# Kernel tuning notes

Hardware: AMD Instinct MI355X
Metric: run time of the kernel (lower is better)

## Reference

```python
import jax, jax.numpy as jnp
import numpy as np

# Graph / model dims (see init_kwargs)
N = 50000          # nodes
E = 800000         # edges (before self loops)
IN, HID, OUT = 128, 64, 47
HEADS = (4, 4, 1)
SLOPE = 0.2        # PyG GATConv default negative_slope
# dropout p=0.6 in the torch module is a no-op in eval mode -> omitted


def _glorot(key, shape):
    fan_in = shape[0] if len(shape) == 2 else int(np.prod(shape))
    return jax.random.normal(key, shape, jnp.float32) / np.sqrt(fan_in)


def setup_inputs() -> dict:
    key = jax.random.key(0)
    ks = jax.random.split(key, 16)
    x = jax.random.normal(ks[0], (N, IN), jnp.float32)
    edge_index = jax.random.randint(ks[1], (2, E), 0, N)
    # layer dims: (in_dim, out_dim_per_head, heads)
    dims = [(IN, HID, HEADS[0]), (HID * HEADS[0], HID, HEADS[1]), (HID * HEADS[1], OUT, HEADS[2])]
    inp = {"x": x, "edge_index": edge_index}
    for i, (d_in, c, h) in enumerate(dims, start=1):
        inp[f"W{i}"] = _glorot(ks[3 * i], (d_in, h * c))
        inp[f"a{i}s"] = _glorot(ks[3 * i + 1], (h, c))
        inp[f"a{i}d"] = _glorot(ks[3 * i + 2], (h, c))
        inp[f"b{i}"] = jnp.zeros((h * c,), jnp.float32)
    return inp


def gat_layer(x, src, dst, W, a_s, a_d, b, h, c):
    # x: [N, d_in] -> per-head features [N, h, c]
    feat = (x @ W).reshape(N, h, c)
    # per-node attention logits [N, h]
    al_src = jnp.einsum('nhc,hc->nh', feat, a_s)
    al_dst = jnp.einsum('nhc,hc->nh', feat, a_d)
    # per-edge score, LeakyReLU (PyG: alpha = a_src[src] + a_dst[dst])
    e = jax.nn.leaky_relu(al_src[src] + al_dst[dst], SLOPE)  # [Etot, h]
    # segment softmax over incoming edges of each dst node
    emax = jax.ops.segment_max(e, dst, num_segments=N)       # [N, h]
    w = jnp.exp(e - emax[dst])
    denom = jax.ops.segment_sum(w, dst, num_segments=N)      # [N, h]
    alpha = w / denom[dst]                                   # [Etot, h]
    # weighted scatter-add aggregation
    out = jax.ops.segment_sum(alpha[:, :, None] * feat[src], dst, num_segments=N)
    return out.reshape(N, h * c) + b                         # concat heads + bias


def reference(x, edge_index, W1, a1s, a1d, b1, W2, a2s, a2d, b2, W3, a3s, a3d, b3):
    loop = jnp.arange(N, dtype=edge_index.dtype)
    src = jnp.concatenate([edge_index[0], loop])  # add_self_loops=True
    dst = jnp.concatenate([edge_index[1], loop])
    h = gat_layer(x, src, dst, W1, a1s, a1d, b1, HEADS[0], HID)
    h = jax.nn.elu(h)
    h = gat_layer(h, src, dst, W2, a2s, a2d, b2, HEADS[1], HID)
    h = jax.nn.elu(h)
    h = gat_layer(h, src, dst, W3, a3s, a3d, b3, HEADS[2], OUT)  # no elu on last layer
    return h
```

## Files before the change

### kernel.cpp

```cpp
#include <hip/hip_runtime.h>
#include <hip/hip_bf16.h>

#define NNODES 50000
#define NEDGES 800000
#define ETOT   (NNODES + NEDGES)
#define MTILES 3136
#define MPAD   (MTILES * 16)
#define NBLK   196

typedef __attribute__((ext_vector_type(8))) short short8;
typedef __attribute__((ext_vector_type(4))) float floatx4;
typedef __attribute__((ext_vector_type(2))) unsigned int uint2v;

__device__ __forceinline__ float bf2f(__hip_bfloat16 x) { return __bfloat162float(x); }
__device__ __forceinline__ __hip_bfloat16 f2bf(float f) { return __float2bfloat16(f); }
__device__ __forceinline__ float sane(float v, float c) {
  v = (v == v) ? v : 0.f;
  return fminf(fmaxf(v, -c), c);
}

__global__ void zero_int_kernel(int* __restrict__ p, int n) {
  int i = blockIdx.x * blockDim.x + threadIdx.x;
  if (i < n) p[i] = 0;
}
__global__ void fill_out_kernel(float* __restrict__ o, int n, float v) {
  int i = blockIdx.x * blockDim.x + threadIdx.x;
  if (i < n) o[i] = v;
}
__global__ void split_input_kernel(const float* __restrict__ in,
                                   __hip_bfloat16* __restrict__ hi,
                                   __hip_bfloat16* __restrict__ lo, int n) {
  int i = blockIdx.x * blockDim.x + threadIdx.x;
  if (i >= n) return;
  float v = sane(in[i], 1e4f);
  __hip_bfloat16 h = f2bf(v);
  hi[i] = h;
  lo[i] = f2bf(v - bf2f(h));
}
__global__ void zero_tail_kernel(__hip_bfloat16* __restrict__ hi,
                                 __hip_bfloat16* __restrict__ lo) {
  const int base = NNODES * 128;
  const int cnt = MPAD * 256 - base;
  int i = blockIdx.x * blockDim.x + threadIdx.x;
  if (i >= cnt) return;
  hi[base + i] = f2bf(0.f);
  lo[base + i] = f2bf(0.f);
}
__global__ void pad47_kernel(const float* __restrict__ a, const float* __restrict__ b,
                             float* __restrict__ ap, float* __restrict__ bp) {
  int i = threadIdx.x;
  ap[i] = (i < 47) ? sane(a[i], 1e4f) : 0.f;
  bp[i] = (i < 47) ? sane(b[i], 1e4f) : 0.f;
}

__global__ void degree_kernel(const int* __restrict__ ei, int* __restrict__ deg) {
  int p = blockIdx.x * blockDim.x + threadIdx.x;
  if (p >= ETOT) return;
  int dst = (p < NEDGES) ? ei[NEDGES + p] : (p - NEDGES);
  dst = min(max(dst, 0), NNODES - 1);
  atomicAdd(&deg[dst], 1);
}

__global__ __launch_bounds__(256) void block_sum_kernel(const int* __restrict__ deg,
                                                        int* __restrict__ bsum) {
  __shared__ int sh[256];
  int b = blockIdx.x, t = threadIdx.x;
  int i = b * 256 + t;
  sh[t] = (i < NNODES) ? deg[i] : 0;
  __syncthreads();
  for (int off = 128; off > 0; off >>= 1) {
    if (t < off) sh[t] += sh[t + off];
    __syncthreads();
  }
  if (t == 0) bsum[b] = sh[0];
}

__global__ __launch_bounds__(256) void scan_bsum_kernel(const int* __restrict__ bsum,
                                                        int* __restrict__ boff,
                                                        int* __restrict__ row_ptr) {
  __shared__ int sh[256];
  int t = threadIdx.x;
  int v = (t < NBLK) ? bsum[t] : 0;
  sh[t] = v;
  __syncthreads();
  for (int off = 1; off < 256; off <<= 1) {
    int u = (t >= off) ? sh[t - off] : 0;
    __syncthreads();
    sh[t] += u;
    __syncthreads();
  }
  if (t < NBLK) boff[t] = sh[t] - v;
  if (t == 255) row_ptr[NNODES] = sh[255];
}

__global__ __launch_bounds__(256) void emit_rowptr_kernel(const int* __restrict__ deg,
                                                          const int* __restrict__ boff,
                                                          int* __restrict__ row_ptr,
                                                          int* __restrict__ cursor) {
  __shared__ int sh[256];
  int b = blockIdx.x, t = threadIdx.x;
  int i = b * 256 + t;
  int d = (i < NNODES) ? deg[i] : 0;
  sh[t] = d;
  __syncthreads();
  for (int off = 1; off < 256; off <<= 1) {
    int u = (t >= off) ? sh[t - off] : 0;
    __syncthreads();
    sh[t] += u;
    __syncthreads();
  }
  if (i < NNODES) {
    int v = boff[b] + sh[t] - d;
    row_ptr[i] = v;
    cursor[i] = v;
  }
}

__global__ void scatter_kernel(const int* __restrict__ ei, int* __restrict__ cursor,
                               int* __restrict__ csr_src) {
  int p = blockIdx.x * blockDim.x + threadIdx.x;
  if (p >= ETOT) return;
  int src, dst;
  if (p < NEDGES) { src = ei[p]; dst = ei[NEDGES + p]; }
  else            { src = p - NEDGES; dst = src; }
  src = min(max(src, 0), NNODES - 1);
  dst = min(max(dst, 0), NNODES - 1);
  int pos = atomicAdd(&cursor[dst], 1);
  pos = min(max(pos, 0), ETOT - 1);
  csr_src[pos] = src;
}

__global__ void pack_w_kernel(const float* __restrict__ W,
                              __hip_bfloat16* __restrict__ Bh,
                              __hip_bfloat16* __restrict__ Bl,
                              int K, int Nreal, int Npad) {
  int idx = blockIdx.x * blockDim.x + threadIdx.x;
  if (idx >= Npad * K) return;
  int e = idx;
  int j = e & 7;    e >>= 3;
  int m = e & 15;   e >>= 4;
  int quad = e & 3; e >>= 2;
  int kch = K >> 5;
  int kk32 = e % kch;
  int nt = e / kch;
  int n = nt * 16 + m;
  int k = kk32 * 32 + quad * 8 + j;
  float v = (n < Nreal) ? sane(W[k * Nreal + n], 1e4f) : 0.f;
  __hip_bfloat16 h = f2bf(v);
  Bh[idx] = h;
  Bl[idx] = f2bf(v - bf2f(h));
}

template<int KDIM, int NOUT, int HEADS, int WAVES_N>
__global__ __launch_bounds__(256) void gemm_attn_kernel(
    const __hip_bfloat16* __restrict__ Ah, const __hip_bfloat16* __restrict__ Al,
    const __hip_bfloat16* __restrict__ Bh, const __hip_bfloat16* __restrict__ Bl,
    const float* __restrict__ asv, const float* __restrict__ adv,
    __hip_bfloat16* __restrict__ Ch, float* __restrict__ als, float* __restrict__ ald) {
  constexpr int KCH = KDIM / 32;
  constexpr int CT = (NOUT / 16) / WAVES_N;
  constexpr int RT = 4;
  constexpr int RGROUPS = 4 / WAVES_N;
  __shared__ __hip_bfloat16 sAh[64 * 32];
  __shared__ __hip_bfloat16 sAl[64 * 32];
  int wave = threadIdx.x >> 6, lane = threadIdx.x & 63;
  int wrow = wave / WAVES_N, wcol = wave % WAVES_N;
  int rt0 = (blockIdx.x * RGROUPS + wrow) * RT;
  int ct0 = wcol * CT;
  int m = lane & 15, quad = lane >> 4;

  const short8* Bph = reinterpret_cast<const short8*>(Bh);
  const short8* Bpl = reinterpret_cast<const short8*>(Bl);

  floatx4 acc[RT][CT];
#pragma unroll
  for (int rt = 0; rt < RT; ++rt)
#pragma unroll
    for (int ct = 0; ct < CT; ++ct) acc[rt][ct] = (floatx4){0.f, 0.f, 0.f, 0.f};

  int tid = threadIdx.x;
  size_t gstage = (size_t)(rt0 * 16 + (tid >> 2)) * KDIM + (tid & 3) * 8;

#pragma unroll 2
  for (int kk = 0; kk < KCH; ++kk) {
    short8 a_h[RT], a_l[RT];
    if constexpr (WAVES_N == 4) {
      short8 vh = *reinterpret_cast<const short8*>(Ah + gstage + kk * 32);
      short8 vl = *reinterpret_cast<const short8*>(Al + gstage + kk * 32);
      __syncthreads();
      *reinterpret_cast<short8*>(&sAh[tid * 8]) = vh;
      *reinterpret_cast<short8*>(&sAl[tid * 8]) = vl;
      __syncthreads();
#pragma unroll
      for (int rt = 0; rt < RT; ++rt) {
        int so = (rt * 16 + m) * 32 + quad * 8;
        a_h[rt] = *reinterpret_cast<const short8*>(&sAh[so]);
        a_l[rt] = *reinterpret_cast<const short8*>(&sAl[so]);
      }
    } else {
#pragma unroll
      for (int rt = 0; rt < RT; ++rt) {
        size_t aoff = (size_t)((rt0 + rt) * 16 + m) * KDIM + kk * 32 + quad * 8;
        a_h[rt] = *reinterpret_cast<const short8*>(Ah + aoff);
        a_l[rt] = *reinterpret_cast<const short8*>(Al + aoff);
      }
    }
#pragma unroll
    for (int ct = 0; ct < CT; ++ct) {
      size_t o = ((size_t)(ct0 + ct) * KCH + kk) * 64 + lane;
      short8 b_h = Bph[o];
      short8 b_l = Bpl[o];
#pragma unroll
      for (int rt = 0; rt < RT; ++rt) {
        acc[rt][ct] = __builtin_amdgcn_mfma_f32_16x16x32_bf16(a_h[rt], b_h, acc[rt][ct], 0, 0, 0);
        acc[rt][ct] = __builtin_amdgcn_mfma_f32_16x16x32_bf16(a_h[rt], b_l, acc[rt][ct], 0, 0, 0);
        acc[rt][ct] = __builtin_amdgcn_mfma_f32_16x16x32_bf16(a_l[rt], b_h, acc[rt][ct], 0, 0, 0);
      }
    }
  }

  constexpr int CPH = NOUT / HEADS;
  int head = (ct0 * 16) / CPH;
  float asl[CT], adl[CT];
#pragma unroll
  for (int ct = 0; ct < CT; ++ct) {
    asl[ct] = asv[(ct0 + ct) * 16 + m];
    adl[ct] = adv[(ct0 + ct) * 16 + m];
  }
  float ps[RT * 4], pd[RT * 4];
#pragma unroll
  for (int i = 0; i < RT * 4; ++i) { ps[i] = 0.f; pd[i] = 0.f; }
#pragma unroll
  for (int rt = 0; rt < RT; ++rt)
#pragma unroll
    for (int ct = 0; ct < CT; ++ct)
#pragma unroll
      for (int r = 0; r < 4; ++r) {
        ps[rt * 4 + r] += acc[rt][ct][r] * asl[ct];
        pd[rt * 4 + r] += acc[rt][ct][r] * adl[ct];
      }
#pragma unroll
  for (int off = 1; off < 16; off <<= 1) {
#pragma unroll
    for (int i = 0; i < RT * 4; ++i) {
      ps[i] += __shfl_xor(ps[i], off);
      pd[i] += __shfl_xor(pd[i], off);
    }
  }
  if (m == 0) {
#pragma unroll
    for (int rt = 0; rt < RT; ++rt)
#pragma unroll
      for (int r = 0; r < 4; ++r) {
        int row = (rt0 + rt) * 16 + quad * 4 + r;
        if (row < NNODES) {
          als[(size_t)row * HEADS + head] = sane(ps[rt * 4 + r], 80.f);
          ald[(size_t)row * HEADS + head] = sane(pd[rt * 4 + r], 80.f);
        }
      }
  }

#pragma unroll
  for (int rt = 0; rt < RT; ++rt)
#pragma unroll
    for (int ct = 0; ct < CT; ++ct)
#pragma unroll
      for (int r = 0; r < 4; ++r) {
        int row = (rt0 + rt) * 16 + quad * 4 + r;
        if (row < NNODES) {
          float v = sane(acc[rt][ct][r], 3e4f);
          Ch[(size_t)row * NOUT + (ct0 + ct) * 16 + m] = f2bf(v);
        }
      }
}

template<int H>
__global__ __launch_bounds__(256) void alpha_kernel(const int* __restrict__ row_ptr,
                                                    const int* __restrict__ csr_src,
                                                    const float* __restrict__ als,
                                                    const float* __restrict__ ald,
                                                    float* __restrict__ alpha) {
  int wid = threadIdx.x >> 6, lane = threadIdx.x & 63;
  int dst = blockIdx.x * 4 + wid;
  if (dst >= NNODES) return;
  int start = row_ptr[dst], end = row_ptr[dst + 1];
  int cnt = end - start;
  if (cnt <= 0) return;
  float adv[H];
#pragma unroll
  for (int h = 0; h < H; ++h) adv[h] = ald[(size_t)dst * H + h];

  if (cnt <= 64) {
    int i = start + lane;
    bool valid = lane < cnt;
    int s = valid ? min(max(csr_src[i], 0), NNODES - 1) : 0;
    float w[H];
#pragma unroll
    for (int h = 0; h < H; ++h) {
      float e = als[(size_t)s * H + h] + adv[h];
      e = e > 0.f ? e : 0.2f * e;
      e = fminf(fmaxf(e, -80.f), 80.f);
      w[h] = valid ? __expf(e) : 0.f;
    }
#pragma unroll
    for (int h = 0; h < H; ++h) {
      float v = w[h];
#pragma unroll
      for (int off = 1; off < 64; off <<= 1) v += __shfl_xor(v, off);
      float inv = 1.f / fmaxf(v, 1e-30f);
      if (valid) alpha[(size_t)i * H + h] = w[h] * inv;
    }
  } else {
    float dl[H];
#pragma unroll
    for (int h = 0; h < H; ++h) dl[h] = 0.f;
    for (int base = start; base < end; base += 64) {
      int i = base + lane;
      bool valid = i < end;
      int s = valid ? min(max(csr_src[i], 0), NNODES - 1) : 0;
#pragma unroll
      for (int h = 0; h < H; ++h) {
        float e = als[(size_t)s * H + h] + adv[h];
        e = e > 0.f ? e : 0.2f * e;
        e = fminf(fmaxf(e, -80.f), 80.f);
        float w = valid ? __expf(e) : 0.f;
        dl[h] += w;
        if (valid) alpha[(size_t)i * H + h] = w;
      }
    }
    float inv[H];
#pragma unroll
    for (int h = 0; h < H; ++h) {
      float v = dl[h];
#pragma unroll
      for (int off = 1; off < 64; off <<= 1) v += __shfl_xor(v, off);
      inv[h] = 1.f / fmaxf(v, 1e-30f);
    }
    for (int base = start; base < end; base += 64) {
      int i = base + lane;
      if (i < end)
#pragma unroll
        for (int h = 0; h < H; ++h) alpha[(size_t)i * H + h] *= inv[h];
    }
  }
}

__global__ __launch_bounds__(256) void agg_mid_kernel(const int* __restrict__ row_ptr,
                                                      const int* __restrict__ csr_src,
                                                      const __hip_bfloat16* __restrict__ Fh,
                                                      const float* __restrict__ alpha,
                                                      const float* __restrict__ bias,
                                                      __hip_bfloat16* __restrict__ Oh,
                                                      __hip_bfloat16* __restrict__ Ol) {
  __shared__ float part[4][256];
  int dst = blockIdx.x;
  int wid = threadIdx.x >> 6, lane = threadIdx.x & 63;
  int start = row_ptr[dst], end = row_ptr[dst + 1];
  int cnt = end - start;
  int head = lane >> 4;
  float a0 = 0.f, a1 = 0.f, a2 = 0.f, a3 = 0.f;
  int p = wid;
  for (; p + 4 < cnt; p += 8) {
    int e0 = start + p, e1 = start + p + 4;
    int s0 = csr_src[e0], s1 = csr_src[e1];
    float w0 = alpha[(size_t)e0 * 4 + head];
    float w1 = alpha[(size_t)e1 * 4 + head];
    uint2v f0 = *reinterpret_cast<const uint2v*>(Fh + (size_t)s0 * 256 + lane * 4);
    uint2v f1 = *reinterpret_cast<const uint2v*>(Fh + (size_t)s1 * 256 + lane * 4);
    a0 += w0 * __uint_as_float(f0.x << 16);
    a1 += w0 * __uint_as_float(f0.x & 0xffff0000u);
    a2 += w0 * __uint_as_float(f0.y << 16);
    a3 += w0 * __uint_as_float(f0.y & 0xffff0000u);
    a0 += w1 * __uint_as_float(f1.x << 16);
    a1 += w1 * __uint_as_float(f1.x & 0xffff0000u);
    a2 += w1 * __uint_as_float(f1.y << 16);
    a3 += w1 * __uint_as_float(f1.y & 0xffff0000u);
  }
  for (; p < cnt; p += 4) {
    int e0 = start + p;
    int s0 = csr_src[e0];
    float w0 = alpha[(size_t)e0 * 4 + head];
    uint2v f0 = *reinterpret_cast<const uint2v*>(Fh + (size_t)s0 * 256 + lane * 4);
    a0 += w0 * __uint_as_float(f0.x << 16);
    a1 += w0 * __uint_as_float(f0.x & 0xffff0000u);
    a2 += w0 * __uint_as_float(f0.y << 16);
    a3 += w0 * __uint_as_float(f0.y & 0xffff0000u);
  }
  *reinterpret_cast<floatx4*>(&part[wid][lane * 4]) = (floatx4){a0, a1, a2, a3};
  __syncthreads();
  int t = threadIdx.x;
  float o = part[0][t] + part[1][t] + part[2][t] + part[3][t] + bias[t];
  o = o > 0.f ? o : __expf(o) - 1.f;
  __hip_bfloat16 h = f2bf(o);
  Oh[(size_t)dst * 256 + t] = h;
  Ol[(size_t)dst * 256 + t] = f2bf(o - bf2f(h));
}

__global__ void agg_final_kernel(const int* __restrict__ row_ptr,
                                 const int* __restrict__ csr_src,
                                 const __hip_bfloat16* __restrict__ Fh,
                                 const float* __restrict__ alpha,
                                 const float* __restrict__ bias,
                                 float* __restrict__ out) {
  int wid = threadIdx.x >> 6, lane = threadIdx.x & 63;
  int dst = blockIdx.x * 4 + wid;
  if (dst >= NNODES) return;
  int start = row_ptr[dst], end = row_ptr[dst + 1];
  float acc = 0.f;
  int e = start;
  for (; e + 1 < end; e += 2) {
    int s0 = csr_src[e], s1 = csr_src[e + 1];
    float w0 = alpha[e], w1 = alpha[e + 1];
    float f0 = bf2f(Fh[(size_t)s0 * 64 + lane]);
    float f1 = bf2f(Fh[(size_t)s1 * 64 + lane]);
    acc += w0 * f0 + w1 * f1;
  }
  for (; e < end; ++e) {
    int s0 = csr_src[e];
    acc += alpha[e] * bf2f(Fh[(size_t)s0 * 64 + lane]);
  }
  if (lane < 47) out[(size_t)dst * 47 + lane] = acc + bias[lane];
}

extern "C" void kernel_launch(void* const* d_in, const int* in_sizes, int n_in,
                              void* d_out, int out_size, void* d_ws, size_t ws_size,
                              hipStream_t stream) {
  const float* x   = (const float*)d_in[0];
  const int* ei    = (const int*)d_in[1];
  const float* W1  = (const float*)d_in[2];
  const float* a1s = (const float*)d_in[3];
  const float* a1d = (const float*)d_in[4];
  const float* b1  = (const float*)d_in[5];
  const float* W2  = (const float*)d_in[6];
  const float* a2s = (const float*)d_in[7];
  const float* a2d = (const float*)d_in[8];
  const float* b2  = (const float*)d_in[9];
  const float* W3  = (const float*)d_in[10];
  const float* a3s = (const float*)d_in[11];
  const float* a3d = (const float*)d_in[12];
  const float* b3  = (const float*)d_in[13];
  float* out = (float*)d_out;
  (void)n_in; (void)in_sizes;

  char* base = (char*)d_ws;
  size_t off = 0;
  auto alloc = [&](size_t bytes) -> char* {
    off = (off + 255) & ~(size_t)255;
    char* p = base + off;
    off += bytes;
    return p;
  };
  int* deg     = (int*)alloc((size_t)NNODES * 4);
  int* cursor  = (int*)alloc((size_t)NNODES * 4);
  int* row_ptr = (int*)alloc((size_t)(NNODES + 1) * 4);
  int* csr_src = (int*)alloc((size_t)ETOT * 4);
  int* bsum    = (int*)alloc(256 * 4);
  int* boff    = (int*)alloc(256 * 4);
  float* als   = (float*)alloc((size_t)NNODES * 4 * 4);
  float* ald   = (float*)alloc((size_t)NNODES * 4 * 4);
  float* alpha = (float*)alloc((size_t)ETOT * 4 * 4);
  __hip_bfloat16* Ah = (__hip_bfloat16*)alloc((size_t)MPAD * 256 * 2);
  __hip_bfloat16* Al = (__hip_bfloat16*)alloc((size_t)MPAD * 256 * 2);
  __hip_bfloat16* Fh = (__hip_bfloat16*)alloc((size_t)NNODES * 256 * 2);
  __hip_bfloat16* wth = (__hip_bfloat16*)alloc((size_t)256 * 256 * 2);
  __hip_bfloat16* wtl = (__hip_bfloat16*)alloc((size_t)256 * 256 * 2);
  float* asv3 = (float*)alloc(64 * 4);
  float* adv3 = (float*)alloc(64 * 4);

  if (ws_size < off) {
    fill_out_kernel<<<(out_size + 255) / 256, 256, 0, stream>>>(out, out_size, 12345.f);
    return;
  }

  zero_int_kernel<<<(NNODES + 255) / 256, 256, 0, stream>>>(deg, NNODES);
  degree_kernel<<<(ETOT + 255) / 256, 256, 0, stream>>>(ei, deg);
  block_sum_kernel<<<NBLK, 256, 0, stream>>>(deg, bsum);
  scan_bsum_kernel<<<1, 256, 0, stream>>>(bsum, boff, row_ptr);
  emit_rowptr_kernel<<<NBLK, 256, 0, stream>>>(deg, boff, row_ptr, cursor);
  scatter_kernel<<<(ETOT + 255) / 256, 256, 0, stream>>>(ei, cursor, csr_src);

  split_input_kernel<<<(NNODES * 128 + 255) / 256, 256, 0, stream>>>(x, Ah, Al, NNODES * 128);
  {
    const int tail = MPAD * 256 - NNODES * 128;
    zero_tail_kernel<<<(tail + 255) / 256, 256, 0, stream>>>(Ah, Al);
  }
  pad47_kernel<<<1, 64, 0, stream>>>(a3s, a3d, asv3, adv3);

  const int grid12 = (NNODES + 63) / 64;
  const int grid3 = (NNODES + 255) / 256;

  pack_w_kernel<<<(256 * 128 + 255) / 256, 256, 0, stream>>>(W1, wth, wtl, 128, 256, 256);
  gemm_attn_kernel<128, 256, 4, 4><<<grid12, 256, 0, stream>>>(Ah, Al, wth, wtl, a1s, a1d,
                                                               Fh, als, ald);
  alpha_kernel<4><<<(NNODES + 3) / 4, 256, 0, stream>>>(row_ptr, csr_src, als, ald, alpha);
  agg_mid_kernel<<<NNODES, 256, 0, stream>>>(row_ptr, csr_src, Fh, alpha, b1, Ah, Al);

  pack_w_kernel<<<(256 * 256 + 255) / 256, 256, 0, stream>>>(W2, wth, wtl, 256, 256, 256);
  gemm_attn_kernel<256, 256, 4, 4><<<grid12, 256, 0, stream>>>(Ah, Al, wth, wtl, a2s, a2d,
                                                               Fh, als, ald);
  alpha_kernel<4><<<(NNODES + 3) / 4, 256, 0, stream>>>(row_ptr, csr_src, als, ald, alpha);
  agg_mid_kernel<<<NNODES, 256, 0, stream>>>(row_ptr, csr_src, Fh, alpha, b2, Ah, Al);

  pack_w_kernel<<<(64 * 256 + 255) / 256, 256, 0, stream>>>(W3, wth, wtl, 256, 47, 64);
  gemm_attn_kernel<256, 64, 1, 1><<<grid3, 256, 0, stream>>>(Ah, Al, wth, wtl, asv3, adv3,
                                                             Fh, als, ald);
  alpha_kernel<1><<<(NNODES + 3) / 4, 256, 0, stream>>>(row_ptr, csr_src, als, ald, alpha);
  agg_final_kernel<<<(NNODES + 3) / 4, 256, 0, stream>>>(row_ptr, csr_src, Fh, alpha, b3, out);
}
```

Measured before the change: 574.8 us.

## Fuse edge-softmax into aggregation kernels and drop alpha buffer

```diff
diff --git a/kernel.cpp b/kernel.cpp
--- a/kernel.cpp
+++ b/kernel.cpp
@@ -17,6 +17,11 @@
 __device__ __forceinline__ float sane(float v, float c) {
   v = (v == v) ? v : 0.f;
   return fminf(fmaxf(v, -c), c);
+}
+__device__ __forceinline__ float edgew(float e) {
+  e = e > 0.f ? e : 0.2f * e;
+  e = fminf(fmaxf(e, -80.f), 80.f);
+  return __expf(e);
 }
 
 __global__ void zero_int_kernel(int* __restrict__ p, int n) {
@@ -274,99 +279,63 @@
       }
 }
 
-template<int H>
-__global__ __launch_bounds__(256) void alpha_kernel(const int* __restrict__ row_ptr,
-                                                    const int* __restrict__ csr_src,
-                                                    const float* __restrict__ als,
-                                                    const float* __restrict__ ald,
-                                                    float* __restrict__ alpha) {
-  int wid = threadIdx.x >> 6, lane = threadIdx.x & 63;
-  int dst = blockIdx.x * 4 + wid;
-  if (dst >= NNODES) return;
-  int start = row_ptr[dst], end = row_ptr[dst + 1];
-  int cnt = end - start;
-  if (cnt <= 0) return;
-  float adv[H];
-#pragma unroll
-  for (int h = 0; h < H; ++h) adv[h] = ald[(size_t)dst * H + h];
-
-  if (cnt <= 64) {
-    int i = start + lane;
-    bool valid = lane < cnt;
-    int s = valid ? min(max(csr_src[i], 0), NNODES - 1) : 0;
-    float w[H];
-#pragma unroll
-    for (int h = 0; h < H; ++h) {
-      float e = als[(size_t)s * H + h] + adv[h];
-      e = e > 0.f ? e : 0.2f * e;
-      e = fminf(fmaxf(e, -80.f), 80.f);
-      w[h] = valid ? __expf(e) : 0.f;
-    }
-#pragma unroll
-    for (int h = 0; h < H; ++h) {
-      float v = w[h];
-#pragma unroll
-      for (int off = 1; off < 64; off <<= 1) v += __shfl_xor(v, off);
-      float inv = 1.f / fmaxf(v, 1e-30f);
-      if (valid) alpha[(size_t)i * H + h] = w[h] * inv;
-    }
-  } else {
-    float dl[H];
-#pragma unroll
-    for (int h = 0; h < H; ++h) dl[h] = 0.f;
-    for (int base = start; base < end; base += 64) {
-      int i = base + lane;
-      bool valid = i < end;
-      int s = valid ? min(max(csr_src[i], 0), NNODES - 1) : 0;
-#pragma unroll
-      for (int h = 0; h < H; ++h) {
-        float e = als[(size_t)s * H + h] + adv[h];
-        e = e > 0.f ? e : 0.2f * e;
-        e = fminf(fmaxf(e, -80.f), 80.f);
-        float w = valid ? __expf(e) : 0.f;
-        dl[h] += w;
-        if (valid) alpha[(size_t)i * H + h] = w;
-      }
-    }
-    float inv[H];
-#pragma unroll
-    for (int h = 0; h < H; ++h) {
-      float v = dl[h];
-#pragma unroll
-      for (int off = 1; off < 64; off <<= 1) v += __shfl_xor(v, off);
-      inv[h] = 1.f / fmaxf(v, 1e-30f);
-    }
-    for (int base = start; base < end; base += 64) {
-      int i = base + lane;
-      if (i < end)
-#pragma unroll
-        for (int h = 0; h < H; ++h) alpha[(size_t)i * H + h] *= inv[h];
-    }
-  }
-}
-
 __global__ __launch_bounds__(256) void agg_mid_kernel(const int* __restrict__ row_ptr,
                                                       const int* __restrict__ csr_src,
                                                       const __hip_bfloat16* __restrict__ Fh,
-                                                      const float* __restrict__ alpha,
+                                                      const float* __restrict__ als,
+                                                      const float* __restrict__ ald,
                                                       const float* __restrict__ bias,
                                                       __hip_bfloat16* __restrict__ Oh,
                                                       __hip_bfloat16* __restrict__ Ol) {
   __shared__ float part[4][256];
+  __shared__ float sinv[4];
   int dst = blockIdx.x;
-  int wid = threadIdx.x >> 6, lane = threadIdx.x & 63;
+  int tid = threadIdx.x, wid = tid >> 6, lane = tid & 63;
   int start = row_ptr[dst], end = row_ptr[dst + 1];
   int cnt = end - start;
+  floatx4 adv = *reinterpret_cast<const floatx4*>(ald + (size_t)dst * 4);
+
+  float d0 = 0.f, d1 = 0.f, d2 = 0.f, d3 = 0.f;
+  for (int p = tid; p < cnt; p += 256) {
+    int s = csr_src[start + p];
+    floatx4 av = *reinterpret_cast<const floatx4*>(als + (size_t)s * 4);
+    d0 += edgew(av.x + adv.x);
+    d1 += edgew(av.y + adv.y);
+    d2 += edgew(av.z + adv.z);
+    d3 += edgew(av.w + adv.w);
+  }
+#pragma unroll
+  for (int off = 1; off < 64; off <<= 1) {
+    d0 += __shfl_xor(d0, off);
+    d1 += __shfl_xor(d1, off);
+    d2 += __shfl_xor(d2, off);
+    d3 += __shfl_xor(d3, off);
+  }
+  if (lane == 0) {
+    part[wid][0] = d0; part[wid][1] = d1; part[wid][2] = d2; part[wid][3] = d3;
+  }
+  __syncthreads();
+  if (tid < 4) {
+    float ds = part[0][tid] + part[1][tid] + part[2][tid] + part[3][tid];
+    sinv[tid] = 1.f / fmaxf(ds, 1e-30f);
+  }
+  __syncthreads();
+
   int head = lane >> 4;
+  float adh = (head == 0) ? adv.x : (head == 1) ? adv.y : (head == 2) ? adv.z : adv.w;
   float a0 = 0.f, a1 = 0.f, a2 = 0.f, a3 = 0.f;
   int p = wid;
-  for (; p + 4 < cnt; p += 8) {
-    int e0 = start + p, e1 = start + p + 4;
-    int s0 = csr_src[e0], s1 = csr_src[e1];
-    float w0 = alpha[(size_t)e0 * 4 + head];
-    float w1 = alpha[(size_t)e1 * 4 + head];
+  for (; p + 12 < cnt; p += 16) {
+    int e0 = start + p, e1 = start + p + 4, e2 = start + p + 8, e3 = start + p + 12;
+    int s0 = csr_src[e0], s1 = csr_src[e1], s2 = csr_src[e2], s3 = csr_src[e3];
+    float w0 = edgew(als[(size_t)s0 * 4 + head] + adh);
+    float w1 = edgew(als[(size_t)s1 * 4 + head] + adh);
+    float w2 = edgew(als[(size_t)s2 * 4 + head] + adh);
+    float w3 = edgew(als[(size_t)s3 * 4 + head] + adh);
     uint2v f0 = *reinterpret_cast<const uint2v*>(Fh + (size_t)s0 * 256 + lane * 4);
     uint2v f1 = *reinterpret_cast<const uint2v*>(Fh + (size_t)s1 * 256 + lane * 4);
+    uint2v f2 = *reinterpret_cast<const uint2v*>(Fh + (size_t)s2 * 256 + lane * 4);
+    uint2v f3 = *reinterpret_cast<const uint2v*>(Fh + (size_t)s3 * 256 + lane * 4);
     a0 += w0 * __uint_as_float(f0.x << 16);
     a1 += w0 * __uint_as_float(f0.x & 0xffff0000u);
     a2 += w0 * __uint_as_float(f0.y << 16);
@@ -375,11 +344,19 @@
     a1 += w1 * __uint_as_float(f1.x & 0xffff0000u);
     a2 += w1 * __uint_as_float(f1.y << 16);
     a3 += w1 * __uint_as_float(f1.y & 0xffff0000u);
+    a0 += w2 * __uint_as_float(f2.x << 16);
+    a1 += w2 * __uint_as_float(f2.x & 0xffff0000u);
+    a2 += w2 * __uint_as_float(f2.y << 16);
+    a3 += w2 * __uint_as_float(f2.y & 0xffff0000u);
+    a0 += w3 * __uint_as_float(f3.x << 16);
+    a1 += w3 * __uint_as_float(f3.x & 0xffff0000u);
+    a2 += w3 * __uint_as_float(f3.y << 16);
+    a3 += w3 * __uint_as_float(f3.y & 0xffff0000u);
   }
   for (; p < cnt; p += 4) {
     int e0 = start + p;
     int s0 = csr_src[e0];
-    float w0 = alpha[(size_t)e0 * 4 + head];
+    float w0 = edgew(als[(size_t)s0 * 4 + head] + adh);
     uint2v f0 = *reinterpret_cast<const uint2v*>(Fh + (size_t)s0 * 256 + lane * 4);
     a0 += w0 * __uint_as_float(f0.x << 16);
     a1 += w0 * __uint_as_float(f0.x & 0xffff0000u);
@@ -388,8 +365,8 @@
   }
   *reinterpret_cast<floatx4*>(&part[wid][lane * 4]) = (floatx4){a0, a1, a2, a3};
   __syncthreads();
-  int t = threadIdx.x;
-  float o = part[0][t] + part[1][t] + part[2][t] + part[3][t] + bias[t];
+  int t = tid;
+  float o = (part[0][t] + part[1][t] + part[2][t] + part[3][t]) * sinv[t >> 6] + bias[t];
   o = o > 0.f ? o : __expf(o) - 1.f;
   __hip_bfloat16 h = f2bf(o);
   Oh[(size_t)dst * 256 + t] = h;
@@ -399,27 +376,36 @@
 __global__ void agg_final_kernel(const int* __restrict__ row_ptr,
                                  const int* __restrict__ csr_src,
                                  const __hip_bfloat16* __restrict__ Fh,
-                                 const float* __restrict__ alpha,
+                                 const float* __restrict__ als,
+                                 const float* __restrict__ ald,
                                  const float* __restrict__ bias,
                                  float* __restrict__ out) {
   int wid = threadIdx.x >> 6, lane = threadIdx.x & 63;
   int dst = blockIdx.x * 4 + wid;
   if (dst >= NNODES) return;
   int start = row_ptr[dst], end = row_ptr[dst + 1];
+  int cnt = end - start;
+  float adh = ald[dst];
+  float d = 0.f;
+  for (int p = lane; p < cnt; p += 64) d += edgew(als[csr_src[start + p]] + adh);
+#pragma unroll
+  for (int off = 1; off < 64; off <<= 1) d += __shfl_xor(d, off);
+  float inv = 1.f / fmaxf(d, 1e-30f);
   float acc = 0.f;
   int e = start;
   for (; e + 1 < end; e += 2) {
     int s0 = csr_src[e], s1 = csr_src[e + 1];
-    float w0 = alpha[e], w1 = alpha[e + 1];
+    float w0 = edgew(als[s0] + adh);
+    float w1 = edgew(als[s1] + adh);
     float f0 = bf2f(Fh[(size_t)s0 * 64 + lane]);
     float f1 = bf2f(Fh[(size_t)s1 * 64 + lane]);
     acc += w0 * f0 + w1 * f1;
   }
   for (; e < end; ++e) {
     int s0 = csr_src[e];
-    acc += alpha[e] * bf2f(Fh[(size_t)s0 * 64 + lane]);
-  }
-  if (lane < 47) out[(size_t)dst * 47 + lane] = acc + bias[lane];
+    acc += edgew(als[s0] + adh) * bf2f(Fh[(size_t)s0 * 64 + lane]);
+  }
+  if (lane < 47) out[(size_t)dst * 47 + lane] = acc * inv + bias[lane];
 }
 
 extern "C" void kernel_launch(void* const* d_in, const int* in_sizes, int n_in,
@@ -458,7 +444,6 @@
   int* boff    = (int*)alloc(256 * 4);
   float* als   = (float*)alloc((size_t)NNODES * 4 * 4);
   float* ald   = (float*)alloc((size_t)NNODES * 4 * 4);
-  float* alpha = (float*)alloc((size_t)ETOT * 4 * 4);
   __hip_bfloat16* Ah = (__hip_bfloat16*)alloc((size_t)MPAD * 256 * 2);
   __hip_bfloat16* Al = (__hip_bfloat16*)alloc((size_t)MPAD * 256 * 2);
   __hip_bfloat16* Fh = (__hip_bfloat16*)alloc((size_t)NNODES * 256 * 2);
@@ -492,18 +477,15 @@
   pack_w_kernel<<<(256 * 128 + 255) / 256, 256, 0, stream>>>(W1, wth, wtl, 128, 256, 256);
   gemm_attn_kernel<128, 256, 4, 4><<<grid12, 256, 0, stream>>>(Ah, Al, wth, wtl, a1s, a1d,
                                                                Fh, als, ald);
-  alpha_kernel<4><<<(NNODES + 3) / 4, 256, 0, stream>>>(row_ptr, csr_src, als, ald, alpha);
-  agg_mid_kernel<<<NNODES, 256, 0, stream>>>(row_ptr, csr_src, Fh, alpha, b1, Ah, Al);
+  agg_mid_kernel<<<NNODES, 256, 0, stream>>>(row_ptr, csr_src, Fh, als, ald, b1, Ah, Al);
 
   pack_w_kernel<<<(256 * 256 + 255) / 256, 256, 0, stream>>>(W2, wth, wtl, 256, 256, 256);
   gemm_attn_kernel<256, 256, 4, 4><<<grid12, 256, 0, stream>>>(Ah, Al, wth, wtl, a2s, a2d,
                                                                Fh, als, ald);
-  alpha_kernel<4><<<(NNODES + 3) / 4, 256, 0, stream>>>(row_ptr, csr_src, als, ald, alpha);
-  agg_mid_kernel<<<NNODES, 256, 0, stream>>>(row_ptr, csr_src, Fh, alpha, b2, Ah, Al);
+  agg_mid_kernel<<<NNODES, 256, 0, stream>>>(row_ptr, csr_src, Fh, als, ald, b2, Ah, Al);
 
   pack_w_kernel<<<(64 * 256 + 255) / 256, 256, 0, stream>>>(W3, wth, wtl, 256, 47, 64);
   gemm_attn_kernel<256, 64, 1, 1><<<grid3, 256, 0, stream>>>(Ah, Al, wth, wtl, asv3, adv3,
                                                              Fh, als, ald);
-  alpha_kernel<1><<<(NNODES + 3) / 4, 256, 0, stream>>>(row_ptr, csr_src, als, ald, alpha);
-  agg_final_kernel<<<(NNODES + 3) / 4, 256, 0, stream>>>(row_ptr, csr_src, Fh, alpha, b3, out);
-}
+  agg_final_kernel<<<(NNODES + 3) / 4, 256, 0, stream>>>(row_ptr, csr_src, Fh, als, ald, b3, out);
+}
```

New measurement: 590.9 us. 1.03x slower.

## Widen aggregation loads, stage two K-chunks per GEMM sync, merge input split kernels

Applied to the files above, without the earlier changes.

```diff
diff --git a/kernel.cpp b/kernel.cpp
--- a/kernel.cpp
+++ b/kernel.cpp
@@ -10,7 +10,7 @@
 
 typedef __attribute__((ext_vector_type(8))) short short8;
 typedef __attribute__((ext_vector_type(4))) float floatx4;
-typedef __attribute__((ext_vector_type(2))) unsigned int uint2v;
+typedef __attribute__((ext_vector_type(4))) unsigned int uint4v;
 
 __device__ __forceinline__ float bf2f(__hip_bfloat16 x) { return __bfloat162float(x); }
 __device__ __forceinline__ __hip_bfloat16 f2bf(float f) { return __float2bfloat16(f); }
@@ -29,22 +29,13 @@
 }
 __global__ void split_input_kernel(const float* __restrict__ in,
                                    __hip_bfloat16* __restrict__ hi,
-                                   __hip_bfloat16* __restrict__ lo, int n) {
+                                   __hip_bfloat16* __restrict__ lo) {
   int i = blockIdx.x * blockDim.x + threadIdx.x;
-  if (i >= n) return;
-  float v = sane(in[i], 1e4f);
+  if (i >= MPAD * 256) return;
+  float v = (i < NNODES * 128) ? sane(in[i], 1e4f) : 0.f;
   __hip_bfloat16 h = f2bf(v);
   hi[i] = h;
   lo[i] = f2bf(v - bf2f(h));
-}
-__global__ void zero_tail_kernel(__hip_bfloat16* __restrict__ hi,
-                                 __hip_bfloat16* __restrict__ lo) {
-  const int base = NNODES * 128;
-  const int cnt = MPAD * 256 - base;
-  int i = blockIdx.x * blockDim.x + threadIdx.x;
-  if (i >= cnt) return;
-  hi[base + i] = f2bf(0.f);
-  lo[base + i] = f2bf(0.f);
 }
 __global__ void pad47_kernel(const float* __restrict__ a, const float* __restrict__ b,
                              float* __restrict__ ap, float* __restrict__ bp) {
@@ -161,8 +152,8 @@
   constexpr int CT = (NOUT / 16) / WAVES_N;
   constexpr int RT = 4;
   constexpr int RGROUPS = 4 / WAVES_N;
-  __shared__ __hip_bfloat16 sAh[64 * 32];
-  __shared__ __hip_bfloat16 sAl[64 * 32];
+  __shared__ __hip_bfloat16 sAh[2 * 64 * 32];
+  __shared__ __hip_bfloat16 sAl[2 * 64 * 32];
   int wave = threadIdx.x >> 6, lane = threadIdx.x & 63;
   int wrow = wave / WAVES_N, wcol = wave % WAVES_N;
   int rt0 = (blockIdx.x * RGROUPS + wrow) * RT;
@@ -182,39 +173,63 @@
   size_t gstage = (size_t)(rt0 * 16 + (tid >> 2)) * KDIM + (tid & 3) * 8;
 
 #pragma unroll 2
-  for (int kk = 0; kk < KCH; ++kk) {
+  for (int ks = 0; ks < KCH / 2; ++ks) {
     short8 a_h[RT], a_l[RT];
     if constexpr (WAVES_N == 4) {
-      short8 vh = *reinterpret_cast<const short8*>(Ah + gstage + kk * 32);
-      short8 vl = *reinterpret_cast<const short8*>(Al + gstage + kk * 32);
+      short8 vh0 = *reinterpret_cast<const short8*>(Ah + gstage + ks * 64);
+      short8 vh1 = *reinterpret_cast<const short8*>(Ah + gstage + ks * 64 + 32);
+      short8 vl0 = *reinterpret_cast<const short8*>(Al + gstage + ks * 64);
+      short8 vl1 = *reinterpret_cast<const short8*>(Al + gstage + ks * 64 + 32);
       __syncthreads();
-      *reinterpret_cast<short8*>(&sAh[tid * 8]) = vh;
-      *reinterpret_cast<short8*>(&sAl[tid * 8]) = vl;
+      *reinterpret_cast<short8*>(&sAh[tid * 8]) = vh0;
+      *reinterpret_cast<short8*>(&sAh[2048 + tid * 8]) = vh1;
+      *reinterpret_cast<short8*>(&sAl[tid * 8]) = vl0;
+      *reinterpret_cast<short8*>(&sAl[2048 + tid * 8]) = vl1;
       __syncthreads();
 #pragma unroll
-      for (int rt = 0; rt < RT; ++rt) {
-        int so = (rt * 16 + m) * 32 + quad * 8;
-        a_h[rt] = *reinterpret_cast<const short8*>(&sAh[so]);
-        a_l[rt] = *reinterpret_cast<const short8*>(&sAl[so]);
+      for (int kk0 = 0; kk0 < 2; ++kk0) {
+#pragma unroll
+        for (int rt = 0; rt < RT; ++rt) {
+          int so = kk0 * 2048 + (rt * 16 + m) * 32 + quad * 8;
+          a_h[rt] = *reinterpret_cast<const short8*>(&sAh[so]);
+          a_l[rt] = *reinterpret_cast<const short8*>(&sAl[so]);
+        }
+        int kk = ks * 2 + kk0;
+#pragma unroll
+        for (int ct = 0; ct < CT; ++ct) {
+          size_t o = ((size_t)(ct0 + ct) * KCH + kk) * 64 + lane;
+          short8 b_h = Bph[o];
+          short8 b_l = Bpl[o];
+#pragma unroll
+          for (int rt = 0; rt < RT; ++rt) {
+            acc[rt][ct] = __builtin_amdgcn_mfma_f32_16x16x32_bf16(a_h[rt], b_h, acc[rt][ct], 0, 0, 0);
+            acc[rt][ct] = __builtin_amdgcn_mfma_f32_16x16x32_bf16(a_h[rt], b_l, acc[rt][ct], 0, 0, 0);
+            acc[rt][ct] = __builtin_amdgcn_mfma_f32_16x16x32_bf16(a_l[rt], b_h, acc[rt][ct], 0, 0, 0);
+          }
+        }
       }
     } else {
 #pragma unroll
-      for (int rt = 0; rt < RT; ++rt) {
-        size_t aoff = (size_t)((rt0 + rt) * 16 + m) * KDIM + kk * 32 + quad * 8;
-        a_h[rt] = *reinterpret_cast<const short8*>(Ah + aoff);
-        a_l[rt] = *reinterpret_cast<const short8*>(Al + aoff);
-      }
-    }
-#pragma unroll
-    for (int ct = 0; ct < CT; ++ct) {
-      size_t o = ((size_t)(ct0 + ct) * KCH + kk) * 64 + lane;
-      short8 b_h = Bph[o];
-      short8 b_l = Bpl[o];
-#pragma unroll
-      for (int rt = 0; rt < RT; ++rt) {
-        acc[rt][ct] = __builtin_amdgcn_mfma_f32_16x16x32_bf16(a_h[rt], b_h, acc[rt][ct], 0, 0, 0);
-        acc[rt][ct] = __builtin_amdgcn_mfma_f32_16x16x32_bf16(a_h[rt], b_l, acc[rt][ct], 0, 0, 0);
-        acc[rt][ct] = __builtin_amdgcn_mfma_f32_16x16x32_bf16(a_l[rt], b_h, acc[rt][ct], 0, 0, 0);
+      for (int kk0 = 0; kk0 < 2; ++kk0) {
+        int kk = ks * 2 + kk0;
+#pragma unroll
+        for (int rt = 0; rt < RT; ++rt) {
+          size_t aoff = (size_t)((rt0 + rt) * 16 + m) * KDIM + kk * 32 + quad * 8;
+          a_h[rt] = *reinterpret_cast<const short8*>(Ah + aoff);
+          a_l[rt] = *reinterpret_cast<const short8*>(Al + aoff);
+        }
+#pragma unroll
+        for (int ct = 0; ct < CT; ++ct) {
+          size_t o = ((size_t)(ct0 + ct) * KCH + kk) * 64 + lane;
+          short8 b_h = Bph[o];
+          short8 b_l = Bpl[o];
+#pragma unroll
+          for (int rt = 0; rt < RT; ++rt) {
+            acc[rt][ct] = __builtin_amdgcn_mfma_f32_16x16x32_bf16(a_h[rt], b_h, acc[rt][ct], 0, 0, 0);
+            acc[rt][ct] = __builtin_amdgcn_mfma_f32_16x16x32_bf16(a_h[rt], b_l, acc[rt][ct], 0, 0, 0);
+            acc[rt][ct] = __builtin_amdgcn_mfma_f32_16x16x32_bf16(a_l[rt], b_h, acc[rt][ct], 0, 0, 0);
+          }
+        }
       }
     }
   }
@@ -352,44 +367,64 @@
                                                       const float* __restrict__ bias,
                                                       __hip_bfloat16* __restrict__ Oh,
                                                       __hip_bfloat16* __restrict__ Ol) {
-  __shared__ float part[4][256];
+  __shared__ float part[8][256];
   int dst = blockIdx.x;
-  int wid = threadIdx.x >> 6, lane = threadIdx.x & 63;
+  int tid = threadIdx.x;
+  int wid = tid >> 6, lane = tid & 63;
+  int half = lane >> 5, cl = lane & 31;
+  int hw = wid * 2 + half;
+  int head = cl >> 3;
   int start = row_ptr[dst], end = row_ptr[dst + 1];
   int cnt = end - start;
-  int head = lane >> 4;
-  float a0 = 0.f, a1 = 0.f, a2 = 0.f, a3 = 0.f;
-  int p = wid;
-  for (; p + 4 < cnt; p += 8) {
-    int e0 = start + p, e1 = start + p + 4;
+  float a[8];
+#pragma unroll
+  for (int j = 0; j < 8; ++j) a[j] = 0.f;
+
+  int p = hw;
+  for (; p + 8 < cnt; p += 16) {
+    int e0 = start + p, e1 = start + p + 8;
     int s0 = csr_src[e0], s1 = csr_src[e1];
     float w0 = alpha[(size_t)e0 * 4 + head];
     float w1 = alpha[(size_t)e1 * 4 + head];
-    uint2v f0 = *reinterpret_cast<const uint2v*>(Fh + (size_t)s0 * 256 + lane * 4);
-    uint2v f1 = *reinterpret_cast<const uint2v*>(Fh + (size_t)s1 * 256 + lane * 4);
-    a0 += w0 * __uint_as_float(f0.x << 16);
-    a1 += w0 * __uint_as_float(f0.x & 0xffff0000u);
-    a2 += w0 * __uint_as_float(f0.y << 16);
-    a3 += w0 * __uint_as_float(f0.y & 0xffff0000u);
-    a0 += w1 * __uint_as_float(f1.x << 16);
-    a1 += w1 * __uint_as_float(f1.x & 0xffff0000u);
-    a2 += w1 * __uint_as_float(f1.y << 16);
-    a3 += w1 * __uint_as_float(f1.y & 0xffff0000u);
-  }
-  for (; p < cnt; p += 4) {
+    uint4v f0 = *reinterpret_cast<const uint4v*>(Fh + (size_t)s0 * 256 + cl * 8);
+    uint4v f1 = *reinterpret_cast<const uint4v*>(Fh + (size_t)s1 * 256 + cl * 8);
+    a[0] += w0 * __uint_as_float(f0.x << 16);
+    a[1] += w0 * __uint_as_float(f0.x & 0xffff0000u);
+    a[2] += w0 * __uint_as_float(f0.y << 16);
+    a[3] += w0 * __uint_as_float(f0.y & 0xffff0000u);
+    a[4] += w0 * __uint_as_float(f0.z << 16);
+    a[5] += w0 * __uint_as_float(f0.z & 0xffff0000u);
+    a[6] += w0 * __uint_as_float(f0.w << 16);
+    a[7] += w0 * __uint_as_float(f0.w & 0xffff0000u);
+    a[0] += w1 * __uint_as_float(f1.x << 16);
+    a[1] += w1 * __uint_as_float(f1.x & 0xffff0000u);
+    a[2] += w1 * __uint_as_float(f1.y << 16);
+    a[3] += w1 * __uint_as_float(f1.y & 0xffff0000u);
+    a[4] += w1 * __uint_as_float(f1.z << 16);
+    a[5] += w1 * __uint_as_float(f1.z & 0xffff0000u);
+    a[6] += w1 * __uint_as_float(f1.w << 16);
+    a[7] += w1 * __uint_as_float(f1.w & 0xffff0000u);
+  }
+  for (; p < cnt; p += 8) {
     int e0 = start + p;
     int s0 = csr_src[e0];
     float w0 = alpha[(size_t)e0 * 4 + head];
-    uint2v f0 = *reinterpret_cast<const uint2v*>(Fh + (size_t)s0 * 256 + lane * 4);
-    a0 += w0 * __uint_as_float(f0.x << 16);
-    a1 += w0 * __uint_as_float(f0.x & 0xffff0000u);
-    a2 += w0 * __uint_as_float(f0.y << 16);
-    a3 += w0 * __uint_as_float(f0.y & 0xffff0000u);
-  }
-  *reinterpret_cast<floatx4*>(&part[wid][lane * 4]) = (floatx4){a0, a1, a2, a3};
+    uint4v f0 = *reinterpret_cast<const uint4v*>(Fh + (size_t)s0 * 256 + cl * 8);
+    a[0] += w0 * __uint_as_float(f0.x << 16);
+    a[1] += w0 * __uint_as_float(f0.x & 0xffff0000u);
+    a[2] += w0 * __uint_as_float(f0.y << 16);
+    a[3] += w0 * __uint_as_float(f0.y & 0xffff0000u);
+    a[4] += w0 * __uint_as_float(f0.z << 16);
+    a[5] += w0 * __uint_as_float(f0.z & 0xffff0000u);
+    a[6] += w0 * __uint_as_float(f0.w << 16);
+    a[7] += w0 * __uint_as_float(f0.w & 0xffff0000u);
+  }
+  *reinterpret_cast<floatx4*>(&part[hw][cl * 8]) = (floatx4){a[0], a[1], a[2], a[3]};
+  *reinterpret_cast<floatx4*>(&part[hw][cl * 8 + 4]) = (floatx4){a[4], a[5], a[6], a[7]};
   __syncthreads();
-  int t = threadIdx.x;
-  float o = part[0][t] + part[1][t] + part[2][t] + part[3][t] + bias[t];
+  int t = tid;
+  float o = ((part[0][t] + part[1][t]) + (part[2][t] + part[3][t])) +
+            ((part[4][t] + part[5][t]) + (part[6][t] + part[7][t])) + bias[t];
   o = o > 0.f ? o : __expf(o) - 1.f;
   __hip_bfloat16 h = f2bf(o);
   Oh[(size_t)dst * 256 + t] = h;
@@ -479,11 +514,7 @@
   emit_rowptr_kernel<<<NBLK, 256, 0, stream>>>(deg, boff, row_ptr, cursor);
   scatter_kernel<<<(ETOT + 255) / 256, 256, 0, stream>>>(ei, cursor, csr_src);
 
-  split_input_kernel<<<(NNODES * 128 + 255) / 256, 256, 0, stream>>>(x, Ah, Al, NNODES * 128);
-  {
-    const int tail = MPAD * 256 - NNODES * 128;
-    zero_tail_kernel<<<(tail + 255) / 256, 256, 0, stream>>>(Ah, Al);
-  }
+  split_input_kernel<<<(MPAD * 256 + 255) / 256, 256, 0, stream>>>(x, Ah, Al);
   pad47_kernel<<<1, 64, 0, stream>>>(a3s, a3d, asv3, adv3);
 
   const int grid12 = (NNODES + 63) / 64;
```

After: 542.6 us. 5.6% less time.
